# Kernel optimization log

Hardware: AMD Instinct MI355X
Metric: run time of the kernel (lower is better)

The kernel has to match this reference:

```python
import jax, jax.numpy as jnp
import numpy as np

D_MODEL = 1024
NUM_HEADS = 16
D_K = D_MODEL // NUM_HEADS


def setup_inputs() -> dict:
    key = jax.random.key(0)
    ks = jax.random.split(key, 11)
    s = 1.0 / np.sqrt(D_MODEL)
    inp = {
        "Q": jax.random.normal(ks[0], (2, 2048, D_MODEL), jnp.float32),
        "K": jax.random.normal(ks[1], (2, 2048, D_MODEL), jnp.float32),
        "V": jax.random.normal(ks[2], (2, 2048, D_MODEL), jnp.float32),
        "W_q": jax.random.uniform(ks[3], (D_MODEL, D_MODEL), jnp.float32, -s, s),
        "b_q": jax.random.uniform(ks[4], (D_MODEL,), jnp.float32, -s, s),
        "W_k": jax.random.uniform(ks[5], (D_MODEL, D_MODEL), jnp.float32, -s, s),
        "b_k": jax.random.uniform(ks[6], (D_MODEL,), jnp.float32, -s, s),
        "W_v": jax.random.uniform(ks[7], (D_MODEL, D_MODEL), jnp.float32, -s, s),
        "b_v": jax.random.uniform(ks[8], (D_MODEL,), jnp.float32, -s, s),
        "W_o": jax.random.uniform(ks[9], (D_MODEL, D_MODEL), jnp.float32, -s, s),
        "b_o": jax.random.uniform(ks[10], (D_MODEL,), jnp.float32, -s, s),
    }
    return inp


def reference(Q, K, V, W_q, b_q, W_k, b_k, W_v, b_v, W_o, b_o):
    B, S, _ = Q.shape
    # Linear projections (torch Linear: x @ W.T + b; W here stored as [in, out])
    q = Q @ W_q + b_q
    k = K @ W_k + b_k
    v = V @ W_v + b_v
    # split heads -> [B, H, S, d_k]
    q = q.reshape(B, S, NUM_HEADS, D_K).transpose(0, 2, 1, 3)
    k = k.reshape(B, S, NUM_HEADS, D_K).transpose(0, 2, 1, 3)
    v = v.reshape(B, S, NUM_HEADS, D_K).transpose(0, 2, 1, 3)
    scale = 1.0 / np.sqrt(D_K).astype(np.float32)
    scores = jnp.einsum('bhqd,bhkd->bhqk', q, k) * scale  # [B,H,S,S]
    probs = jax.nn.softmax(scores, axis=-1)
    attn = jnp.einsum('bhqk,bhkd->bhqd', probs, v)  # [B,H,S,d_k]
    attn = attn.transpose(0, 2, 1, 3).reshape(B, S, D_MODEL)
    return attn @ W_o + b_o
```

## Files before the change

kernel.cpp:

```cpp
#include <hip/hip_runtime.h>
#include <math.h>

#define SEQ   2048
#define DM    1024
#define NH    16
#define DK    64
#define MTOT  4096
#define QSCALE 0.18033688011112043f

typedef __bf16 bf16x8 __attribute__((ext_vector_type(8)));
typedef float  f32x4  __attribute__((ext_vector_type(4)));
typedef unsigned short u16;
typedef unsigned long long u64;

__device__ __forceinline__ u16 f2bf(float f) {
    unsigned int u = __float_as_uint(f);
    u += 0x7fff + ((u >> 16) & 1);
    return (u16)(u >> 16);
}

__device__ __forceinline__ void async16(const void* g, void* l) {
    __builtin_amdgcn_global_load_lds(
        (const __attribute__((address_space(1))) unsigned int*)(unsigned long long)g,
        (__attribute__((address_space(3))) unsigned int*)(unsigned int)(unsigned long long)l,
        16, 0, 0);
}

__device__ __forceinline__ bf16x8 ld16(const u16* p) {
    bf16x8 v;
    __builtin_memcpy(&v, p, 16);
    return v;
}
__device__ __forceinline__ void st8(u16* p, unsigned int lo, unsigned int hi) {
    u64 q = ((u64)hi << 32) | lo;
    __builtin_memcpy(p, &q, 8);
}

__global__ __launch_bounds__(256)
void cvt_in(const float* __restrict__ Q, const float* __restrict__ K,
            const float* __restrict__ V, u16* __restrict__ Qb,
            u16* __restrict__ Kb, u16* __restrict__ Vb)
{
    const float* src; u16* dst;
    if (blockIdx.z == 0)      { src = Q; dst = Qb; }
    else if (blockIdx.z == 1) { src = K; dst = Kb; }
    else                      { src = V; dst = Vb; }
    const size_t i = ((size_t)blockIdx.x * 256 + threadIdx.x) * 8;
    float4 a = *(const float4*)&src[i];
    float4 b = *(const float4*)&src[i + 4];
    uint4 o;
    o.x = (unsigned)f2bf(a.x) | ((unsigned)f2bf(a.y) << 16);
    o.y = (unsigned)f2bf(a.z) | ((unsigned)f2bf(a.w) << 16);
    o.z = (unsigned)f2bf(b.x) | ((unsigned)f2bf(b.y) << 16);
    o.w = (unsigned)f2bf(b.z) | ((unsigned)f2bf(b.w) << 16);
    *(uint4*)&dst[i] = o;
}

__global__ __launch_bounds__(256)
void cvt_wt(const float* __restrict__ Wq, const float* __restrict__ Wk,
            const float* __restrict__ Wv, const float* __restrict__ Wo,
            u16* __restrict__ Tq, u16* __restrict__ Tk,
            u16* __restrict__ Tv, u16* __restrict__ To)
{
    const float* W; u16* Wt;
    if (blockIdx.z == 0)      { W = Wq; Wt = Tq; }
    else if (blockIdx.z == 1) { W = Wk; Wt = Tk; }
    else if (blockIdx.z == 2) { W = Wv; Wt = Tv; }
    else                      { W = Wo; Wt = To; }
    __shared__ float Ts[64][65];
    const int t = threadIdx.x;
    const int k0 = blockIdx.x * 64, n0 = blockIdx.y * 64;
#pragma unroll
    for (int p = 0; p < 4; ++p) {
        const int flat = t + p * 256;
        const int r = flat >> 4, c4 = (flat & 15) * 4;
        float4 v = *(const float4*)&W[(size_t)(k0 + r) * DM + n0 + c4];
        Ts[r][c4 + 0] = v.x; Ts[r][c4 + 1] = v.y;
        Ts[r][c4 + 2] = v.z; Ts[r][c4 + 3] = v.w;
    }
    __syncthreads();
#pragma unroll
    for (int p = 0; p < 2; ++p) {
        const int flat = t + p * 256;
        const int n = flat >> 3, kc = (flat & 7) * 8;
        uint4 o;
        o.x = (unsigned)f2bf(Ts[kc + 0][n]) | ((unsigned)f2bf(Ts[kc + 1][n]) << 16);
        o.y = (unsigned)f2bf(Ts[kc + 2][n]) | ((unsigned)f2bf(Ts[kc + 3][n]) << 16);
        o.z = (unsigned)f2bf(Ts[kc + 4][n]) | ((unsigned)f2bf(Ts[kc + 5][n]) << 16);
        o.w = (unsigned)f2bf(Ts[kc + 6][n]) | ((unsigned)f2bf(Ts[kc + 7][n]) << 16);
        *(uint4*)&Wt[(size_t)(n0 + n) * DM + k0 + kc] = o;
    }
}

template <int SCATTER>
__device__ __forceinline__ void gemm_core(const u16* __restrict__ A,
                                          const u16* __restrict__ Wt,
                                          const float* __restrict__ bias,
                                          void* __restrict__ Out, float scale)
{
    __shared__ u16 As[128 * 32];
    __shared__ u16 Bs[128 * 32];

    const int tid = threadIdx.x;
    const int lane = tid & 63;
    const int wv = __builtin_amdgcn_readfirstlane(tid >> 6);
    const int wm = wv >> 1, wn = wv & 1;
    const int lane15 = lane & 15, quad = lane >> 4;
    const int row0 = blockIdx.x * 128, col0 = blockIdx.y * 128;

    const int arow = lane >> 2;
    const int acol = (lane & 3) * 8;

    f32x4 acc[4][4];
#pragma unroll
    for (int i = 0; i < 4; ++i)
#pragma unroll
        for (int j = 0; j < 4; ++j) acc[i][j] = (f32x4)0.f;

    for (int k0 = 0; k0 < DM; k0 += 32) {
#pragma unroll
        for (int cc = 0; cc < 2; ++cc) {
            const int c = 2 * wv + cc;
            async16(&A[(size_t)(row0 + c * 16 + arow) * DM + k0 + acol],
                    &As[c * 512]);
            async16(&Wt[(size_t)(col0 + c * 16 + arow) * DM + k0 + acol],
                    &Bs[c * 512]);
        }
        __syncthreads();

        bf16x8 af[4];
#pragma unroll
        for (int mi = 0; mi < 4; ++mi)
            af[mi] = ld16(&As[(wm * 64 + mi * 16 + lane15) * 32 + quad * 8]);
#pragma unroll
        for (int ni = 0; ni < 4; ++ni) {
            bf16x8 bfrag = ld16(&Bs[(wn * 64 + ni * 16 + lane15) * 32 + quad * 8]);
#pragma unroll
            for (int mi = 0; mi < 4; ++mi)
                acc[mi][ni] = __builtin_amdgcn_mfma_f32_16x16x32_bf16(
                    af[mi], bfrag, acc[mi][ni], 0, 0, 0);
        }
        __syncthreads();
    }

#pragma unroll
    for (int mi = 0; mi < 4; ++mi) {
        const int mbase = row0 + wm * 64 + mi * 16 + quad * 4;
#pragma unroll
        for (int ni = 0; ni < 4; ++ni) {
            const int n = col0 + wn * 64 + ni * 16 + lane15;
            const float bz = bias[n];
            if (SCATTER == 1) {
                const int h = n >> 6, dk = n & 63;
#pragma unroll
                for (int r = 0; r < 4; ++r) {
                    const int mm = mbase + r;
                    const int b_ = mm >> 11, s = mm & 2047;
                    ((u16*)Out)[(((size_t)(b_ * NH + h)) * SEQ + s) * DK + dk] =
                        f2bf((acc[mi][ni][r] + bz) * scale);
                }
            } else if (SCATTER == 2) {
                const int h = n >> 6, dk = n & 63;
                const int b_ = mbase >> 11, s0 = mbase & 2047;
                u64 q = (u64)f2bf((acc[mi][ni][0] + bz) * scale)
                      | ((u64)f2bf((acc[mi][ni][1] + bz) * scale) << 16)
                      | ((u64)f2bf((acc[mi][ni][2] + bz) * scale) << 32)
                      | ((u64)f2bf((acc[mi][ni][3] + bz) * scale) << 48);
                u16* dst = (u16*)Out +
                    (((size_t)(b_ * NH + h)) * DK + dk) * SEQ + s0;
                __builtin_memcpy(dst, &q, 8);
            } else {
#pragma unroll
                for (int r = 0; r < 4; ++r) {
                    const int mm = mbase + r;
                    ((float*)Out)[(size_t)mm * DM + n] = acc[mi][ni][r] + bz;
                }
            }
        }
    }
}

__global__ __launch_bounds__(256)
void qkv_gemm(const u16* __restrict__ Qb, const u16* __restrict__ Kb,
              const u16* __restrict__ Vb,
              const u16* __restrict__ Tq, const u16* __restrict__ Tk,
              const u16* __restrict__ Tv,
              const float* __restrict__ bq, const float* __restrict__ bk,
              const float* __restrict__ bv,
              u16* __restrict__ qw, u16* __restrict__ kw, u16* __restrict__ vtw)
{
    if (blockIdx.z == 0)      gemm_core<1>(Qb, Tq, bq, qw, QSCALE);
    else if (blockIdx.z == 1) gemm_core<1>(Kb, Tk, bk, kw, 1.0f);
    else                      gemm_core<2>(Vb, Tv, bv, vtw, 1.0f);
}

__global__ __launch_bounds__(256)
void out_gemm(const u16* __restrict__ A, const u16* __restrict__ Wt,
              const float* __restrict__ bias, float* __restrict__ Out)
{
    __shared__ u16 As[128 * 32];
    __shared__ u16 Bs[64 * 32];

    const int tid = threadIdx.x;
    const int lane = tid & 63;
    const int wv = __builtin_amdgcn_readfirstlane(tid >> 6);
    const int wm = wv >> 1, wn = wv & 1;
    const int lane15 = lane & 15, quad = lane >> 4;
    const int row0 = blockIdx.x * 128, col0 = blockIdx.y * 64;

    const int arow = lane >> 2;
    const int acol = (lane & 3) * 8;

    f32x4 acc[4][2];
#pragma unroll
    for (int i = 0; i < 4; ++i)
#pragma unroll
        for (int j = 0; j < 2; ++j) acc[i][j] = (f32x4)0.f;

    for (int k0 = 0; k0 < DM; k0 += 32) {
#pragma unroll
        for (int cc = 0; cc < 2; ++cc) {
            const int c = 2 * wv + cc;
            async16(&A[(size_t)(row0 + c * 16 + arow) * DM + k0 + acol],
                    &As[c * 512]);
        }
        async16(&Wt[(size_t)(col0 + wv * 16 + arow) * DM + k0 + acol],
                &Bs[wv * 512]);
        __syncthreads();

        bf16x8 af[4];
#pragma unroll
        for (int mi = 0; mi < 4; ++mi)
            af[mi] = ld16(&As[(wm * 64 + mi * 16 + lane15) * 32 + quad * 8]);
#pragma unroll
        for (int ni = 0; ni < 2; ++ni) {
            bf16x8 bfrag = ld16(&Bs[(wn * 32 + ni * 16 + lane15) * 32 + quad * 8]);
#pragma unroll
            for (int mi = 0; mi < 4; ++mi)
                acc[mi][ni] = __builtin_amdgcn_mfma_f32_16x16x32_bf16(
                    af[mi], bfrag, acc[mi][ni], 0, 0, 0);
        }
        __syncthreads();
    }

#pragma unroll
    for (int mi = 0; mi < 4; ++mi) {
        const int mbase = row0 + wm * 64 + mi * 16 + quad * 4;
#pragma unroll
        for (int ni = 0; ni < 2; ++ni) {
            const int n = col0 + wn * 32 + ni * 16 + lane15;
            const float bz = bias[n];
#pragma unroll
            for (int r = 0; r < 4; ++r)
                Out[(size_t)(mbase + r) * DM + n] = acc[mi][ni][r] + bz;
        }
    }
}

__global__ __launch_bounds__(256, 4)
void attn_mfma(const u16* __restrict__ qw, const u16* __restrict__ kw,
               const u16* __restrict__ vt, u16* __restrict__ opart,
               float* __restrict__ lw)
{
    __shared__ u16 Ks[2][64 * 72];
    __shared__ u16 Vts[2][64 * 72];

    const int tid = threadIdx.x;
    const int lane = tid & 63;
    const int wv = tid >> 6;
    const int lane15 = lane & 15, quad = lane >> 4;

    const int flat = blockIdx.x;
    const int xcd = flat & 7;
    const int rest = flat >> 3;
    const int bh = xcd * 4 + (rest & 3);
    const int qt = (rest >> 2) & 15;
    const int ks = rest >> 6;
    const int q0 = qt * 128;
    const int c0beg = ks * 1024;
    const size_t base = (size_t)bh * SEQ * DK;

    bf16x8 qb[2][2];
#pragma unroll
    for (int mi = 0; mi < 2; ++mi)
#pragma unroll
        for (int kk = 0; kk < 2; ++kk)
            qb[mi][kk] = ld16(&qw[base +
                (size_t)(q0 + wv * 32 + mi * 16 + lane15) * DK + kk * 32 + quad * 8]);

    f32x4 o_acc[2][4];
    float lpart[2];
#pragma unroll
    for (int mi = 0; mi < 2; ++mi) {
        lpart[mi] = 0.f;
#pragma unroll
        for (int nd = 0; nd < 4; ++nd) o_acc[mi][nd] = (f32x4)0.f;
    }

    const int sr = tid >> 2;
    const int sh = (tid & 3) * 16;

    int vslot[2];
#pragma unroll
    for (int j = 0; j < 2; ++j) {
        const int c8 = sh + j * 8;
        const int a = c8 >> 4, b = (c8 >> 2) & 3;
        vslot[j] = (a >> 1) * 32 + b * 8 + (a & 1) * 4;
    }

#pragma unroll
    for (int j = 0; j < 2; ++j) {
        const int c8 = sh + j * 8;
        uint4 kv = *(const uint4*)&kw[base + (size_t)(c0beg + sr) * DK + c8];
        st8(&Ks[0][sr * 72 + c8], kv.x, kv.y);
        st8(&Ks[0][sr * 72 + c8 + 4], kv.z, kv.w);
        uint4 vv = *(const uint4*)&vt[base + (size_t)sr * SEQ + c0beg + c8];
        st8(&Vts[0][sr * 72 + vslot[j]], vv.x, vv.y);
        st8(&Vts[0][sr * 72 + vslot[j] + 8], vv.z, vv.w);
    }
    __syncthreads();

    for (int it = 0; it < 16; ++it) {
        const int cur = it & 1;
        const u16* Kc = &Ks[cur][0];
        const u16* Vc = &Vts[cur][0];

        uint4 kpre[2], vpre[2];
        const bool more = (it < 15);
        if (more) {
            const int cn = c0beg + (it + 1) * 64;
#pragma unroll
            for (int j = 0; j < 2; ++j) {
                const int c8 = sh + j * 8;
                kpre[j] = *(const uint4*)&kw[base + (size_t)(cn + sr) * DK + c8];
                vpre[j] = *(const uint4*)&vt[base + (size_t)sr * SEQ + cn + c8];
            }
        }

        f32x4 sT[2][4];
#pragma unroll
        for (int mi = 0; mi < 2; ++mi)
#pragma unroll
            for (int ki = 0; ki < 4; ++ki) sT[mi][ki] = (f32x4)0.f;
        __builtin_amdgcn_s_setprio(1);
#pragma unroll
        for (int ki = 0; ki < 4; ++ki)
#pragma unroll
            for (int kk = 0; kk < 2; ++kk) {
                bf16x8 ka = ld16(&Kc[(ki * 16 + lane15) * 72 + kk * 32 + quad * 8]);
#pragma unroll
                for (int mi = 0; mi < 2; ++mi)
                    sT[mi][ki] = __builtin_amdgcn_mfma_f32_16x16x32_bf16(
                        ka, qb[mi][kk], sT[mi][ki], 0, 0, 0);
            }
        __builtin_amdgcn_s_setprio(0);

        bf16x8 pa[2][2];
#pragma unroll
        for (int mi = 0; mi < 2; ++mi) {
            unsigned int ulo[4], uhi[4];
#pragma unroll
            for (int ki = 0; ki < 4; ++ki) {
                unsigned int u[4];
#pragma unroll
                for (int r = 0; r < 4; ++r) {
                    const float p = __builtin_amdgcn_exp2f(sT[mi][ki][r]);
                    lpart[mi] += p;
                    u[r] = __float_as_uint(p) + 0x8000u;
                }
                ulo[ki] = __builtin_amdgcn_perm(u[1], u[0], 0x07060302u);
                uhi[ki] = __builtin_amdgcn_perm(u[3], u[2], 0x07060302u);
            }
#pragma unroll
            for (int kk = 0; kk < 2; ++kk) {
                union { uint4 u; bf16x8 v; } pk;
                pk.u.x = ulo[2 * kk];     pk.u.y = uhi[2 * kk];
                pk.u.z = ulo[2 * kk + 1]; pk.u.w = uhi[2 * kk + 1];
                pa[mi][kk] = pk.v;
            }
        }

        __builtin_amdgcn_s_setprio(1);
#pragma unroll
        for (int nd = 0; nd < 4; ++nd)
#pragma unroll
            for (int kk = 0; kk < 2; ++kk) {
                bf16x8 vb = ld16(&Vc[(nd * 16 + lane15) * 72 + kk * 32 + quad * 8]);
#pragma unroll
                for (int mi = 0; mi < 2; ++mi)
                    o_acc[mi][nd] = __builtin_amdgcn_mfma_f32_16x16x32_bf16(
                        pa[mi][kk], vb, o_acc[mi][nd], 0, 0, 0);
            }
        __builtin_amdgcn_s_setprio(0);

        if (more) {
            const int nxt = cur ^ 1;
#pragma unroll
            for (int j = 0; j < 2; ++j) {
                const int c8 = sh + j * 8;
                st8(&Ks[nxt][sr * 72 + c8], kpre[j].x, kpre[j].y);
                st8(&Ks[nxt][sr * 72 + c8 + 4], kpre[j].z, kpre[j].w);
                st8(&Vts[nxt][sr * 72 + vslot[j]], vpre[j].x, vpre[j].y);
                st8(&Vts[nxt][sr * 72 + vslot[j] + 8], vpre[j].z, vpre[j].w);
            }
        }
        __syncthreads();
    }

    const size_t rowbase = (size_t)(ks * 32 + bh) * SEQ;
#pragma unroll
    for (int mi = 0; mi < 2; ++mi) {
        float l = lpart[mi];
        l += __shfl_xor(l, 16);
        l += __shfl_xor(l, 32);
        if (quad == 0)
            lw[rowbase + q0 + wv * 32 + mi * 16 + lane15] = l;
    }
#pragma unroll
    for (int mi = 0; mi < 2; ++mi)
#pragma unroll
        for (int r = 0; r < 4; ++r) {
            const int s = q0 + wv * 32 + mi * 16 + quad * 4 + r;
#pragma unroll
            for (int nd = 0; nd < 4; ++nd)
                opart[(rowbase + s) * DK + nd * 16 + lane15] = f2bf(o_acc[mi][nd][r]);
        }
}

__global__ __launch_bounds__(256)
void attn_combine(const u16* __restrict__ opart, const float* __restrict__ lw,
                  u16* __restrict__ attnb)
{
    const int flat = blockIdx.x * 256 + threadIdx.x;
    const int dv = (flat & 7) * 8;
    const int s  = (flat >> 3) & 2047;
    const int bh = flat >> 14;
    const size_t i0 = ((size_t)bh * SEQ + s) * DK + dv;
    const size_t i1 = i0 + (size_t)32 * SEQ * DK;
    uint4 a = *(const uint4*)&opart[i0];
    uint4 b = *(const uint4*)&opart[i1];
    const float l = lw[(size_t)bh * SEQ + s] + lw[(size_t)(32 + bh) * SEQ + s];
    const float inv = 1.f / l;
    unsigned int au[4] = {a.x, a.y, a.z, a.w};
    unsigned int bu[4] = {b.x, b.y, b.z, b.w};
    unsigned int ou[4];
#pragma unroll
    for (int j = 0; j < 4; ++j) {
        const float e0 = __uint_as_float(au[j] << 16) + __uint_as_float(bu[j] << 16);
        const float e1 = __uint_as_float(au[j] & 0xffff0000u) +
                         __uint_as_float(bu[j] & 0xffff0000u);
        ou[j] = (unsigned)f2bf(e0 * inv) | ((unsigned)f2bf(e1 * inv) << 16);
    }
    const int b_ = bh >> 4, h = bh & 15;
    uint4 o; o.x = ou[0]; o.y = ou[1]; o.z = ou[2]; o.w = ou[3];
    *(uint4*)&attnb[((size_t)b_ * SEQ + s) * DM + h * DK + dv] = o;
}

extern "C" void kernel_launch(void* const* d_in, const int* in_sizes, int n_in,
                              void* d_out, int out_size, void* d_ws, size_t ws_size,
                              hipStream_t stream)
{
    const float* Q  = (const float*)d_in[0];
    const float* K  = (const float*)d_in[1];
    const float* V  = (const float*)d_in[2];
    const float* Wq = (const float*)d_in[3];
    const float* bq = (const float*)d_in[4];
    const float* Wk = (const float*)d_in[5];
    const float* bk = (const float*)d_in[6];
    const float* Wv = (const float*)d_in[7];
    const float* bv = (const float*)d_in[8];
    const float* Wo = (const float*)d_in[9];
    const float* bo = (const float*)d_in[10];
    float* out = (float*)d_out;

    const size_t MB = 1024 * 1024;
    char* w8 = (char*)d_ws;
    u16* Qbf = (u16*)(w8 + 0 * MB);
    u16* Kbf = (u16*)(w8 + 8 * MB);
    u16* Vbf = (u16*)(w8 + 16 * MB);
    u16* Wtq = (u16*)(w8 + 24 * MB);
    u16* Wtk = (u16*)(w8 + 26 * MB);
    u16* Wtv = (u16*)(w8 + 28 * MB);
    u16* Wto = (u16*)(w8 + 30 * MB);
    u16* qw  = (u16*)(w8 + 32 * MB);
    u16* kw  = (u16*)(w8 + 40 * MB);
    u16* vtw = (u16*)(w8 + 48 * MB);
    u16* opart = Kbf;
    float* lwb = (float*)(w8 + 56 * MB);
    u16* attnb = Qbf;

    cvt_in<<<dim3(2048, 1, 3), 256, 0, stream>>>(Q, K, V, Qbf, Kbf, Vbf);
    cvt_wt<<<dim3(16, 16, 4), 256, 0, stream>>>(Wq, Wk, Wv, Wo,
                                                Wtq, Wtk, Wtv, Wto);
    qkv_gemm<<<dim3(32, 8, 3), 256, 0, stream>>>(Qbf, Kbf, Vbf, Wtq, Wtk, Wtv,
                                                 bq, bk, bv, qw, kw, vtw);
    attn_mfma<<<1024, 256, 0, stream>>>(qw, kw, vtw, opart, lwb);
    attn_combine<<<2048, 256, 0, stream>>>(opart, lwb, attnb);
    out_gemm<<<dim3(32, 16), 256, 0, stream>>>(attnb, Wto, bo, out);
}
```

Measured before the change: 223.7 us.

## Split attention keys four ways, swizzle LDS tiles, raise occupancy hint

The attention kernel now splits the key dimension into four 512-key chunks instead of two, doubling the grid to 2048 blocks so there are more waves to fill the GPU. The padded 72-stride LDS layout is replaced by an XOR-swizzled 64-stride layout, which shrinks shared memory and allows a launch_bounds hint of 5 blocks per CU. The combine kernel now sums four bf16 partials and four row sums, and workspace buffers are remapped to hold the larger partial output. The trade-off is more partial-output traffic and combine work in exchange for better parallelism and occupancy.

```diff
diff --git a/kernel.cpp b/kernel.cpp
--- a/kernel.cpp
+++ b/kernel.cpp
@@ -34,6 +34,10 @@
 __device__ __forceinline__ void st8(u16* p, unsigned int lo, unsigned int hi) {
     u64 q = ((u64)hi << 32) | lo;
     __builtin_memcpy(p, &q, 8);
+}
+
+__device__ __forceinline__ int swz(int row, int col) {
+    return (row * 64 + col) ^ ((row & 7) << 3);
 }
 
 __global__ __launch_bounds__(256)
@@ -257,13 +261,13 @@
     }
 }
 
-__global__ __launch_bounds__(256, 4)
+__global__ __launch_bounds__(256, 5)
 void attn_mfma(const u16* __restrict__ qw, const u16* __restrict__ kw,
                const u16* __restrict__ vt, u16* __restrict__ opart,
                float* __restrict__ lw)
 {
-    __shared__ u16 Ks[2][64 * 72];
-    __shared__ u16 Vts[2][64 * 72];
+    __shared__ u16 Ks[2][64 * 64];
+    __shared__ u16 Vts[2][64 * 64];
 
     const int tid = threadIdx.x;
     const int lane = tid & 63;
@@ -277,7 +281,7 @@
     const int qt = (rest >> 2) & 15;
     const int ks = rest >> 6;
     const int q0 = qt * 128;
-    const int c0beg = ks * 1024;
+    const int c0beg = ks * 512;
     const size_t base = (size_t)bh * SEQ * DK;
 
     bf16x8 qb[2][2];
@@ -312,21 +316,21 @@
     for (int j = 0; j < 2; ++j) {
         const int c8 = sh + j * 8;
         uint4 kv = *(const uint4*)&kw[base + (size_t)(c0beg + sr) * DK + c8];
-        st8(&Ks[0][sr * 72 + c8], kv.x, kv.y);
-        st8(&Ks[0][sr * 72 + c8 + 4], kv.z, kv.w);
+        st8(&Ks[0][swz(sr, c8)], kv.x, kv.y);
+        st8(&Ks[0][swz(sr, c8 + 4)], kv.z, kv.w);
         uint4 vv = *(const uint4*)&vt[base + (size_t)sr * SEQ + c0beg + c8];
-        st8(&Vts[0][sr * 72 + vslot[j]], vv.x, vv.y);
-        st8(&Vts[0][sr * 72 + vslot[j] + 8], vv.z, vv.w);
+        st8(&Vts[0][swz(sr, vslot[j])], vv.x, vv.y);
+        st8(&Vts[0][swz(sr, vslot[j] + 8)], vv.z, vv.w);
     }
     __syncthreads();
 
-    for (int it = 0; it < 16; ++it) {
+    for (int it = 0; it < 8; ++it) {
         const int cur = it & 1;
         const u16* Kc = &Ks[cur][0];
         const u16* Vc = &Vts[cur][0];
 
         uint4 kpre[2], vpre[2];
-        const bool more = (it < 15);
+        const bool more = (it < 7);
         if (more) {
             const int cn = c0beg + (it + 1) * 64;
 #pragma unroll
@@ -347,7 +351,7 @@
         for (int ki = 0; ki < 4; ++ki)
 #pragma unroll
             for (int kk = 0; kk < 2; ++kk) {
-                bf16x8 ka = ld16(&Kc[(ki * 16 + lane15) * 72 + kk * 32 + quad * 8]);
+                bf16x8 ka = ld16(&Kc[swz(ki * 16 + lane15, kk * 32 + quad * 8)]);
 #pragma unroll
                 for (int mi = 0; mi < 2; ++mi)
                     sT[mi][ki] = __builtin_amdgcn_mfma_f32_16x16x32_bf16(
@@ -385,7 +389,7 @@
         for (int nd = 0; nd < 4; ++nd)
 #pragma unroll
             for (int kk = 0; kk < 2; ++kk) {
-                bf16x8 vb = ld16(&Vc[(nd * 16 + lane15) * 72 + kk * 32 + quad * 8]);
+                bf16x8 vb = ld16(&Vc[swz(nd * 16 + lane15, kk * 32 + quad * 8)]);
 #pragma unroll
                 for (int mi = 0; mi < 2; ++mi)
                     o_acc[mi][nd] = __builtin_amdgcn_mfma_f32_16x16x32_bf16(
@@ -398,10 +402,10 @@
 #pragma unroll
             for (int j = 0; j < 2; ++j) {
                 const int c8 = sh + j * 8;
-                st8(&Ks[nxt][sr * 72 + c8], kpre[j].x, kpre[j].y);
-                st8(&Ks[nxt][sr * 72 + c8 + 4], kpre[j].z, kpre[j].w);
-                st8(&Vts[nxt][sr * 72 + vslot[j]], vpre[j].x, vpre[j].y);
-                st8(&Vts[nxt][sr * 72 + vslot[j] + 8], vpre[j].z, vpre[j].w);
+                st8(&Ks[nxt][swz(sr, c8)], kpre[j].x, kpre[j].y);
+                st8(&Ks[nxt][swz(sr, c8 + 4)], kpre[j].z, kpre[j].w);
+                st8(&Vts[nxt][swz(sr, vslot[j])], vpre[j].x, vpre[j].y);
+                st8(&Vts[nxt][swz(sr, vslot[j] + 8)], vpre[j].z, vpre[j].w);
             }
         }
         __syncthreads();
@@ -435,22 +439,34 @@
     const int dv = (flat & 7) * 8;
     const int s  = (flat >> 3) & 2047;
     const int bh = flat >> 14;
+    const size_t stride = (size_t)32 * SEQ * DK;
     const size_t i0 = ((size_t)bh * SEQ + s) * DK + dv;
-    const size_t i1 = i0 + (size_t)32 * SEQ * DK;
-    uint4 a = *(const uint4*)&opart[i0];
-    uint4 b = *(const uint4*)&opart[i1];
-    const float l = lw[(size_t)bh * SEQ + s] + lw[(size_t)(32 + bh) * SEQ + s];
+
+    float l = 0.f;
+#pragma unroll
+    for (int p = 0; p < 4; ++p)
+        l += lw[(size_t)(p * 32 + bh) * SEQ + s];
     const float inv = 1.f / l;
-    unsigned int au[4] = {a.x, a.y, a.z, a.w};
-    unsigned int bu[4] = {b.x, b.y, b.z, b.w};
+
+    float e[8];
+#pragma unroll
+    for (int j = 0; j < 8; ++j) e[j] = 0.f;
+#pragma unroll
+    for (int p = 0; p < 4; ++p) {
+        uint4 a = *(const uint4*)&opart[i0 + p * stride];
+        unsigned int au[4] = {a.x, a.y, a.z, a.w};
+#pragma unroll
+        for (int j = 0; j < 4; ++j) {
+            e[2 * j]     += __uint_as_float(au[j] << 16);
+            e[2 * j + 1] += __uint_as_float(au[j] & 0xffff0000u);
+        }
+    }
     unsigned int ou[4];
 #pragma unroll
-    for (int j = 0; j < 4; ++j) {
-        const float e0 = __uint_as_float(au[j] << 16) + __uint_as_float(bu[j] << 16);
-        const float e1 = __uint_as_float(au[j] & 0xffff0000u) +
-                         __uint_as_float(bu[j] & 0xffff0000u);
-        ou[j] = (unsigned)f2bf(e0 * inv) | ((unsigned)f2bf(e1 * inv) << 16);
-    }
+    for (int j = 0; j < 4; ++j)
+        ou[j] = (unsigned)f2bf(e[2 * j] * inv) |
+                ((unsigned)f2bf(e[2 * j + 1] * inv) << 16);
+
     const int b_ = bh >> 4, h = bh & 15;
     uint4 o; o.x = ou[0]; o.y = ou[1]; o.z = ou[2]; o.w = ou[3];
     *(uint4*)&attnb[((size_t)b_ * SEQ + s) * DM + h * DK + dv] = o;
@@ -481,20 +497,20 @@
     u16* Wtq = (u16*)(w8 + 24 * MB);
     u16* Wtk = (u16*)(w8 + 26 * MB);
     u16* Wtv = (u16*)(w8 + 28 * MB);
-    u16* Wto = (u16*)(w8 + 30 * MB);
     u16* qw  = (u16*)(w8 + 32 * MB);
     u16* kw  = (u16*)(w8 + 40 * MB);
     u16* vtw = (u16*)(w8 + 48 * MB);
-    u16* opart = Kbf;
     float* lwb = (float*)(w8 + 56 * MB);
-    u16* attnb = Qbf;
+    u16* Wto = (u16*)(w8 + 57 * MB);
+    u16* opart = Qbf;
+    u16* attnb = qw;
 
     cvt_in<<<dim3(2048, 1, 3), 256, 0, stream>>>(Q, K, V, Qbf, Kbf, Vbf);
     cvt_wt<<<dim3(16, 16, 4), 256, 0, stream>>>(Wq, Wk, Wv, Wo,
                                                 Wtq, Wtk, Wtv, Wto);
     qkv_gemm<<<dim3(32, 8, 3), 256, 0, stream>>>(Qbf, Kbf, Vbf, Wtq, Wtk, Wtv,
                                                  bq, bk, bv, qw, kw, vtw);
-    attn_mfma<<<1024, 256, 0, stream>>>(qw, kw, vtw, opart, lwb);
+    attn_mfma<<<2048, 256, 0, stream>>>(qw, kw, vtw, opart, lwb);
     attn_combine<<<2048, 256, 0, stream>>>(opart, lwb, attnb);
     out_gemm<<<dim3(32, 16), 256, 0, stream>>>(attnb, Wto, bo, out);
 }
```

New measurement: 398.9 us. 1.78x slower.
